# Kernel tuning notes

Hardware: AMD Instinct MI355X
Metric: run time of the kernel (lower is better)

Reference implementation:

```python
import jax, jax.numpy as jnp
import numpy as np

WH, WW = 7, 7
N = WH * WW
DIM = 384
HEADS = 12
NW = 64          # windows per image
B_ = 2048        # batch * NW


def _relative_position_index():
    ch, cw = np.meshgrid(np.arange(WH), np.arange(WW), indexing='ij')
    coords = np.stack([ch, cw]).reshape(2, -1)                      # [2, N]
    rel = coords[:, :, None] - coords[:, None, :]                   # [2, N, N]
    rel = rel.transpose(1, 2, 0)
    rel[:, :, 0] += WH - 1
    rel[:, :, 1] += WW - 1
    rel[:, :, 0] *= 2 * WW - 1
    return jnp.asarray(rel.sum(-1), dtype=jnp.int32)                # [N, N]


def setup_inputs() -> dict:
    key = jax.random.key(0)
    ks = jax.random.split(key, 7)
    return {
        'x': jax.random.normal(ks[0], (B_, N, DIM), dtype=jnp.float32),
        'qkv_w': jax.random.normal(ks[1], (3 * DIM, DIM), dtype=jnp.float32) * 0.02,
        'qkv_b': jax.random.normal(ks[2], (3 * DIM,), dtype=jnp.float32) * 0.02,
        'proj_w': jax.random.normal(ks[3], (DIM, DIM), dtype=jnp.float32) * 0.02,
        'proj_b': jax.random.normal(ks[4], (DIM,), dtype=jnp.float32) * 0.02,
        'bias_table': jax.random.normal(ks[5], ((2 * WH - 1) * (2 * WW - 1), HEADS), dtype=jnp.float32) * 0.02,
        'mask': jax.random.normal(ks[6], (NW, N, N), dtype=jnp.float32),
        'rel_idx': _relative_position_index(),
    }


def reference(x, qkv_w, qkv_b, proj_w, proj_b, bias_table, mask, rel_idx):
    B_, n, C = x.shape
    H = HEADS
    hd = C // H
    scale = hd ** (-0.5)

    qkv = x @ qkv_w.T + qkv_b                                        # [B_, N, 3C]
    qkv = qkv.reshape(B_, n, 3, H, hd).transpose(2, 0, 3, 1, 4)      # [3, B_, H, N, hd]
    q, k, v = qkv[0], qkv[1], qkv[2]

    attn = jnp.einsum('bhqd,bhkd->bhqk', q * scale, k)               # [B_, H, N, N]

    rpb = bias_table[rel_idx.reshape(-1)].reshape(n, n, H)           # gather [N, N, H]
    attn = attn + rpb.transpose(2, 0, 1)[None]                       # [B_, H, N, N]

    nW = mask.shape[0]
    attn = attn.reshape(B_ // nW, nW, H, n, n) + mask[None, :, None]
    attn = attn.reshape(B_, H, n, n)
    attn = jax.nn.softmax(attn, axis=-1)

    out = jnp.einsum('bhqk,bhkd->bhqd', attn, v)                     # [B_, H, N, hd]
    out = out.transpose(0, 2, 1, 3).reshape(B_, n, C)
    return out @ proj_w.T + proj_b
```

## Files before the change

kernel.cpp:

```cpp
#include <hip/hip_runtime.h>
#include <hip/hip_bf16.h>
#include <cstdint>
#include <cstddef>

#define NTOK 49
#define DIM 384
#define KDIM 384
#define HEADS 12
#define HD 32
#define BATCH 2048
#define MROWS (BATCH * NTOK)

typedef unsigned short u16;
typedef __bf16 bf16x8 __attribute__((ext_vector_type(8)));
typedef unsigned short u16x8 __attribute__((ext_vector_type(8)));
typedef float f32x4 __attribute__((ext_vector_type(4)));

__device__ __forceinline__ u16 f2b(float f) {
  union { float f; unsigned u; } v; v.f = f;
  unsigned r = v.u + 0x7fffu + ((v.u >> 16) & 1u);
  return (u16)(r >> 16);
}

__device__ __forceinline__ bf16x8 ld_bf8(const u16* p) {
  u16x8 u = *(const u16x8*)p;
  return __builtin_bit_cast(bf16x8, u);
}

__device__ __forceinline__ void gload_lds16(const void* g, void* l) {
  __builtin_amdgcn_global_load_lds(
      (const __attribute__((address_space(1))) unsigned*)g,
      (__attribute__((address_space(3))) unsigned*)l, 16, 0, 0);
}

__global__ __launch_bounds__(256) void k_prep(const float* __restrict__ x,
                                              u16* __restrict__ xb,
                                              const float* __restrict__ qkv_w,
                                              u16* __restrict__ wqkvb,
                                              const float* __restrict__ proj_w,
                                              u16* __restrict__ wprojb,
                                              const float* __restrict__ bias_table,
                                              const float* __restrict__ mask,
                                              const int* __restrict__ rel_idx,
                                              float* __restrict__ rpbm) {
  int blk = blockIdx.x;
  if (blk < 38208) {
    const float* in;
    u16* out;
    int i;
    if (blk < 37632) {
      in = x; out = xb; i = blk * 256 + threadIdx.x;
    } else if (blk < 38064) {
      in = qkv_w; out = wqkvb; i = (blk - 37632) * 256 + threadIdx.x;
    } else {
      in = proj_w; out = wprojb; i = (blk - 38064) * 256 + threadIdx.x;
    }
    float4 v = ((const float4*)in)[i];
    ushort4 o;
    o.x = f2b(v.x); o.y = f2b(v.y); o.z = f2b(v.z); o.w = f2b(v.w);
    ((ushort4*)out)[i] = o;
  } else {
    int idx = (blk - 38208) * 256 + threadIdx.x;
    int r  = idx & 3;
    int l  = (idx >> 2) & 63;
    int ni = (idx >> 8) & 3;
    int mi = (idx >> 10) & 3;
    int w  = (idx >> 12) & 63;
    int h  = idx >> 18;
    int kk = mi * 16 + (l >> 4) * 4 + r;
    int qq = ni * 16 + (l & 15);
    float v = -1e30f;
    if (kk < NTOK && qq < NTOK)
      v = bias_table[rel_idx[qq * NTOK + kk] * HEADS + h] +
          mask[(w * NTOK + qq) * NTOK + kk];
    rpbm[idx] = v;
  }
}

template <int OUT_BF16, int NCOLS, int NTN, int GD8>
__global__ __launch_bounds__(512, 4) void k_gemm256(const u16* __restrict__ A,
                                                    const u16* __restrict__ B,
                                                    const float* __restrict__ bias,
                                                    void* __restrict__ Cv) {
  __shared__ u16 sh[36864];
  int bid = blockIdx.x;
  int tile = (bid & 7) * GD8 + (bid >> 3);
  int mt = tile / NTN, nt = tile - mt * NTN;
  long m0 = (long)mt * 256;
  int n0 = nt * 128;
  int tid = threadIdx.x;
  int lane = tid & 63, wid = tid >> 6;
  int wr = (wid >> 1) * 64, wc = (wid & 1) * 64;
  int c = lane & 15, g = lane >> 4;
  int gsw = (g ^ ((c >> 1) & 3)) * 8;

  int srow = wid * 16 + (lane >> 2);
  int scol = ((lane & 3) ^ ((lane >> 3) & 3)) * 8;
  const u16* gA = A + (m0 + srow) * (long)KDIM + scol;
  const u16* gB = B + (long)(n0 + srow) * KDIM + scol;
  int lrow = srow, lseg = (lane & 3) * 8;

  f32x4 acc[4][4] = {};
  bf16x8 af[4], bfr[4];

#define STAGE256(BUF, KT)                                                      \
  {                                                                            \
    u16* As_ = sh + (BUF) * 12288;                                             \
    u16* Bs_ = As_ + 8192;                                                     \
    gload_lds16(gA + (KT), &As_[lrow * 32 + lseg]);                            \
    gload_lds16(gA + (KT) + 128L * KDIM, &As_[(lrow + 128) * 32 + lseg]);      \
    gload_lds16(gB + (KT), &Bs_[lrow * 32 + lseg]);                            \
  }

#define FRAGREAD(BUF)                                                          \
  {                                                                            \
    const u16* As = sh + (BUF) * 12288;                                        \
    const u16* Bs = As + 8192;                                                 \
    _Pragma("unroll") for (int i = 0; i < 4; ++i) {                            \
      af[i]  = ld_bf8(&As[(wr + i * 16 + c) * 32 + gsw]);                      \
      bfr[i] = ld_bf8(&Bs[(wc + i * 16 + c) * 32 + gsw]);                      \
    }                                                                          \
  }

#define MFMA_CL                                                                \
  __builtin_amdgcn_s_setprio(1);                                               \
  _Pragma("unroll") for (int mi = 0; mi < 4; ++mi)                             \
  _Pragma("unroll") for (int ni = 0; ni < 4; ++ni)                             \
      acc[mi][ni] = __builtin_amdgcn_mfma_f32_16x16x32_bf16(                   \
          af[mi], bfr[ni], acc[mi][ni], 0, 0, 0);                              \
  __builtin_amdgcn_s_setprio(0);

#define GITER(T, NV)                                                           \
  {                                                                            \
    MFMA_CL;                                                                   \
    asm volatile("s_waitcnt vmcnt(" #NV ")" ::: "memory");                     \
    __builtin_amdgcn_s_barrier();                                              \
    __builtin_amdgcn_sched_barrier(0);                                         \
    if ((T) + 3 < 12) STAGE256((T) % 3, ((T) + 3) * 32);                       \
    FRAGREAD(((T) + 1) % 3);                                                   \
  }

  STAGE256(0, 0);
  STAGE256(1, 32);
  STAGE256(2, 64);
  asm volatile("s_waitcnt vmcnt(6)" ::: "memory");
  __builtin_amdgcn_s_barrier();
  __builtin_amdgcn_sched_barrier(0);
  FRAGREAD(0);

  GITER(0, 3)  GITER(1, 3)  GITER(2, 3)  GITER(3, 3)
  GITER(4, 3)  GITER(5, 3)  GITER(6, 3)  GITER(7, 3)
  GITER(8, 3)  GITER(9, 3)  GITER(10, 0)
  { MFMA_CL; }
  __builtin_amdgcn_s_barrier();
#undef GITER
#undef MFMA_CL
#undef FRAGREAD
#undef STAGE256

  if (OUT_BF16) {
    u16* C = (u16*)Cv;
#pragma unroll
    for (int mi = 0; mi < 4; ++mi)
#pragma unroll
      for (int ni = 0; ni < 4; ++ni) {
        int col = wc + ni * 16 + c;
        float bv = bias[n0 + col];
#pragma unroll
        for (int r = 0; r < 4; ++r) {
          int row = wr + mi * 16 + g * 4 + r;
          sh[row * 128 + col] = f2b(acc[mi][ni][r] + bv);
        }
      }
    __syncthreads();
#pragma unroll
    for (int rep = 0; rep < 8; ++rep) {
      int idx = rep * 4096 + tid * 8;
      int row = idx >> 7, col = idx & 127;
      *(u16x8*)(C + (m0 + row) * NCOLS + n0 + col) = *(const u16x8*)&sh[idx];
    }
  } else {
    float* C = (float*)Cv;
    float* shf = (float*)sh;
#pragma unroll
    for (int chunk = 0; chunk < 2; ++chunk) {
      __syncthreads();
      if ((wid >> 2) == chunk) {
#pragma unroll
        for (int mi = 0; mi < 4; ++mi)
#pragma unroll
          for (int ni = 0; ni < 4; ++ni) {
            int col = wc + ni * 16 + c;
            float bv = bias[n0 + col];
#pragma unroll
            for (int r = 0; r < 4; ++r) {
              int lr = ((wid >> 1) & 1) * 64 + mi * 16 + g * 4 + r;
              shf[lr * 128 + col] = acc[mi][ni][r] + bv;
            }
          }
      }
      __syncthreads();
#pragma unroll
      for (int rep = 0; rep < 8; ++rep) {
        int idx = rep * 2048 + tid * 4;
        int row = idx >> 7, col = idx & 127;
        *(float4*)(C + (m0 + chunk * 128 + row) * NCOLS + n0 + col) =
            *(const float4*)&shf[idx];
      }
    }
  }
}

__global__ __launch_bounds__(256) void k_attn(const u16* __restrict__ qkv,
                                              const float* __restrict__ rpbmT,
                                              u16* __restrict__ attnout) {
  __shared__ u16 P_lds[4][64 * 64];
  __shared__ u16 vT_lds[4][32 * 64];
  int lane = threadIdx.x & 63, wid = threadIdx.x >> 6;
  int blk = blockIdx.x;
  int w = blk / 96;
  int rr = blk - w * 96;
  int j = rr / 3;
  int hb = rr - j * 3;
  int b = j * 64 + w;
  int h = hb * 4 + wid;
  const u16* base = qkv + (size_t)b * (NTOK * 1152);
  int c = lane & 15, g = lane >> 4;

  u16* vt = vT_lds[wid];
  {
    const u16* vbase = base + 2 * DIM + h * HD;
#pragma unroll
    for (int t = 0; t < 4; ++t) {
      int idx = t * 64 + lane;
      int jj = idx >> 2, d0 = (idx & 3) * 8;
      int jr = jj < NTOK ? jj : NTOK - 1;
      u16x8 vv = *(const u16x8*)(vbase + (size_t)jr * 1152 + d0);
#pragma unroll
      for (int dd = 0; dd < 8; ++dd) {
        int d = d0 + dd;
        int byte = (d * 128 + jj * 2) ^ ((d & 7) << 4);
        *(u16*)((char*)vt + byte) = (u16)vv[dd];
      }
    }
  }

  bf16x8 kf[4], qf[4];
#pragma unroll
  for (int mi = 0; mi < 4; ++mi) {
    int row = mi * 16 + c; if (row > NTOK - 1) row = NTOK - 1;
    kf[mi] = ld_bf8(base + (size_t)row * 1152 + DIM + h * HD + g * 8);
  }
#pragma unroll
  for (int nj = 0; nj < 4; ++nj) {
    int row = nj * 16 + c; if (row > NTOK - 1) row = NTOK - 1;
    qf[nj] = ld_bf8(base + (size_t)row * 1152 + h * HD + g * 8);
  }

  f32x4 s[4][4];
  f32x4 zf = {0.f, 0.f, 0.f, 0.f};
#pragma unroll
  for (int mi = 0; mi < 4; ++mi)
#pragma unroll
    for (int nj = 0; nj < 4; ++nj)
      s[mi][nj] = __builtin_amdgcn_mfma_f32_16x16x32_bf16(kf[mi], qf[nj], zf,
                                                          0, 0, 0);

  const float scale = 0.17677669529663687f;
  const f32x4* rp = (const f32x4*)(rpbmT + ((size_t)(h * 64 + w)) * 4096);
#pragma unroll
  for (int mi = 0; mi < 4; ++mi)
#pragma unroll
    for (int nj = 0; nj < 4; ++nj) {
      f32x4 rv = rp[(mi * 4 + nj) * 64 + lane];
#pragma unroll
      for (int r = 0; r < 4; ++r)
        s[mi][nj][r] = s[mi][nj][r] * scale + rv[r];
    }

  float inv[4];
#pragma unroll
  for (int nj = 0; nj < 4; ++nj) {
    float mx = s[0][nj][0];
#pragma unroll
    for (int mi = 0; mi < 4; ++mi)
#pragma unroll
      for (int r = 0; r < 4; ++r)
        mx = fmaxf(mx, s[mi][nj][r]);
    mx = fmaxf(mx, __shfl_xor(mx, 16));
    mx = fmaxf(mx, __shfl_xor(mx, 32));
    float sum = 0.f;
#pragma unroll
    for (int mi = 0; mi < 4; ++mi)
#pragma unroll
      for (int r = 0; r < 4; ++r) {
        float p = __expf(s[mi][nj][r] - mx);
        s[mi][nj][r] = p;
        sum += p;
      }
    sum += __shfl_xor(sum, 16);
    sum += __shfl_xor(sum, 32);
    inv[nj] = __builtin_amdgcn_rcpf(sum);
  }

  u16* pl = P_lds[wid];
#pragma unroll
  for (int mi = 0; mi < 4; ++mi)
#pragma unroll
    for (int nj = 0; nj < 4; ++nj) {
      unsigned w0, w1;
      asm("v_cvt_pk_bf16_f32 %0, %1, %2"
          : "=v"(w0) : "v"(s[mi][nj][0]), "v"(s[mi][nj][1]));
      asm("v_cvt_pk_bf16_f32 %0, %1, %2"
          : "=v"(w1) : "v"(s[mi][nj][2]), "v"(s[mi][nj][3]));
      int q = nj * 16 + c;
      int byte = (q * 128 + (mi * 16 + g * 4) * 2) ^ ((c & 7) << 4);
      uint2 val; val.x = w0; val.y = w1;
      *(uint2*)((char*)pl + byte) = val;
    }
  asm volatile("s_waitcnt lgkmcnt(0)" ::: "memory");
  __builtin_amdgcn_sched_barrier(0);

  f32x4 o[2][4] = {};
#pragma unroll
  for (int ks = 0; ks < 2; ++ks) {
    bf16x8 vb[2];
#pragma unroll
    for (int mi2 = 0; mi2 < 2; ++mi2) {
      int d = mi2 * 16 + c;
      int byte = (d * 128 + ks * 64 + g * 16) ^ ((d & 7) << 4);
      vb[mi2] = __builtin_bit_cast(bf16x8, *(const u16x8*)((const char*)vt + byte));
    }
#pragma unroll
    for (int nj = 0; nj < 4; ++nj) {
      int q = nj * 16 + c;
      int byte = (q * 128 + (ks * 32 + g * 8) * 2) ^ ((c & 7) << 4);
      bf16x8 pb = __builtin_bit_cast(bf16x8, *(const u16x8*)((const char*)pl + byte));
#pragma unroll
      for (int mi2 = 0; mi2 < 2; ++mi2)
        o[mi2][nj] = __builtin_amdgcn_mfma_f32_16x16x32_bf16(vb[mi2], pb,
                                                             o[mi2][nj], 0, 0, 0);
    }
  }

  u16* obase = attnout + (size_t)b * (NTOK * DIM) + h * HD;
#pragma unroll
  for (int mi2 = 0; mi2 < 2; ++mi2)
#pragma unroll
    for (int nj = 0; nj < 4; ++nj) {
      int q = nj * 16 + c;
      if (q < NTOK) {
#pragma unroll
        for (int r = 0; r < 4; ++r)
          obase[(size_t)q * DIM + mi2 * 16 + g * 4 + r] =
              f2b(o[mi2][nj][r] * inv[nj]);
      }
    }
}

extern "C" void kernel_launch(void* const* d_in, const int* in_sizes, int n_in,
                              void* d_out, int out_size, void* d_ws, size_t ws_size,
                              hipStream_t stream) {
  const float* x       = (const float*)d_in[0];
  const float* qkv_w   = (const float*)d_in[1];
  const float* qkv_b   = (const float*)d_in[2];
  const float* proj_w  = (const float*)d_in[3];
  const float* proj_b  = (const float*)d_in[4];
  const float* bias_tb = (const float*)d_in[5];
  const float* mask    = (const float*)d_in[6];
  const int*   rel_idx = (const int*)d_in[7];
  float* out = (float*)d_out;

  char* ws = (char*)d_ws;
  u16*   xb      = (u16*)(ws + 0);
  u16*   wqkvb   = (u16*)(ws + 77070336);
  u16*   wprojb  = (u16*)(ws + 77955072);
  float* rpbm    = (float*)(ws + 78249984);
  u16*   qkv     = (u16*)(ws + 90832896);
  u16*   attnout = (u16*)(ws + 322043904);

  k_prep<<<50496, 256, 0, stream>>>(x, xb, qkv_w, wqkvb, proj_w, wprojb,
                                    bias_tb, mask, rel_idx, rpbm);

  k_gemm256<1, 1152, 9, 441><<<3528, 512, 0, stream>>>(xb, wqkvb, qkv_b,
                                                       (void*)qkv);

  k_attn<<<6144, 256, 0, stream>>>(qkv, rpbm, attnout);

  k_gemm256<0, 384, 3, 147><<<1176, 512, 0, stream>>>(attnout, wprojb, proj_b,
                                                      (void*)out);

  (void)in_sizes; (void)n_in; (void)out_size; (void)ws_size;
}
```

Before: 341.7 us.

## Restructure GEMM main loop into 64-wide K tiles with quarter-phased double buffering

Replaces the 3-stage 32-wide K pipeline in the shared GEMM kernel with a 2-buffer, 64-wide K pipeline. Each K step is split into four quadrant phases of MFMA work, and the next tile's global-to-LDS loads are interleaved between phases with extra barriers. The LDS footprint grows and launch bounds drop to 2 blocks per CU, trading occupancy and added barriers for fewer loop iterations and finer overlap of loads with compute. The XOR swizzle is updated to match the 64-element row.

```diff
diff --git a/kernel.cpp b/kernel.cpp
--- a/kernel.cpp
+++ b/kernel.cpp
@@ -78,11 +78,11 @@
 }
 
 template <int OUT_BF16, int NCOLS, int NTN, int GD8>
-__global__ __launch_bounds__(512, 4) void k_gemm256(const u16* __restrict__ A,
-                                                    const u16* __restrict__ B,
-                                                    const float* __restrict__ bias,
-                                                    void* __restrict__ Cv) {
-  __shared__ u16 sh[36864];
+__global__ __launch_bounds__(512, 2) void k_gemm8p(const u16* __restrict__ A,
+                                                   const u16* __restrict__ B,
+                                                   const float* __restrict__ bias,
+                                                   void* __restrict__ Cv) {
+  __shared__ u16 sh[49152];
   int bid = blockIdx.x;
   int tile = (bid & 7) * GD8 + (bid >> 3);
   int mt = tile / NTN, nt = tile - mt * NTN;
@@ -92,71 +92,89 @@
   int lane = tid & 63, wid = tid >> 6;
   int wr = (wid >> 1) * 64, wc = (wid & 1) * 64;
   int c = lane & 15, g = lane >> 4;
-  int gsw = (g ^ ((c >> 1) & 3)) * 8;
-
-  int srow = wid * 16 + (lane >> 2);
-  int scol = ((lane & 3) ^ ((lane >> 3) & 3)) * 8;
-  const u16* gA = A + (m0 + srow) * (long)KDIM + scol;
-  const u16* gB = B + (long)(n0 + srow) * KDIM + scol;
-  int lrow = srow, lseg = (lane & 3) * 8;
+  int r8 = lane >> 3;
+  int sg = ((lane & 7) ^ r8) * 8;
+  const u16* gAb = A + (m0 + r8) * (long)KDIM + sg;
+  const u16* gBb = B + (long)(n0 + r8) * KDIM + sg;
+  int a_l0 = wid * 32;
+  int b_l0 = wid * 16;
 
   f32x4 acc[4][4] = {};
-  bf16x8 af[4], bfr[4];
-
-#define STAGE256(BUF, KT)                                                      \
+
+#define STA(BUF, KT, Q)                                                        \
+  gload_lds16(gAb + (long)(a_l0 + (Q) * 8) * KDIM + (KT),                      \
+              &sh[(BUF) * 24576 + (a_l0 + (Q) * 8) * 64] + lane * 8);
+#define STB(BUF, KT, Q)                                                        \
+  gload_lds16(gBb + (long)(b_l0 + (Q) * 8) * KDIM + (KT),                      \
+              &sh[(BUF) * 24576 + 16384 + (b_l0 + (Q) * 8) * 64] + lane * 8);
+
+#define READQ(BUF, MI0, NI0)                                                   \
+  const u16* As = sh + (BUF) * 24576;                                          \
+  const u16* Bs = As + 16384;                                                  \
+  bf16x8 aq[2][2], bq[2][2];                                                   \
+  _Pragma("unroll") for (int i = 0; i < 2; ++i) {                              \
+    int R = wr + ((MI0) + i) * 16 + c;                                         \
+    int S = wc + ((NI0) + i) * 16 + c;                                         \
+    _Pragma("unroll") for (int kk = 0; kk < 2; ++kk) {                         \
+      aq[i][kk] = ld_bf8(&As[R * 64 + (((kk * 4 + g) ^ (R & 7)) * 8)]);        \
+      bq[i][kk] = ld_bf8(&Bs[S * 64 + (((kk * 4 + g) ^ (S & 7)) * 8)]);        \
+    }                                                                          \
+  }
+
+#define MFMAQ(MI0, NI0)                                                        \
+  __builtin_amdgcn_s_setprio(1);                                               \
+  _Pragma("unroll") for (int kk = 0; kk < 2; ++kk)                             \
+  _Pragma("unroll") for (int i = 0; i < 2; ++i)                                \
+  _Pragma("unroll") for (int jj = 0; jj < 2; ++jj)                             \
+    acc[(MI0) + i][(NI0) + jj] = __builtin_amdgcn_mfma_f32_16x16x32_bf16(      \
+        aq[i][kk], bq[jj][kk], acc[(MI0) + i][(NI0) + jj], 0, 0, 0);           \
+  __builtin_amdgcn_s_setprio(0);
+
+#define GK(T, NV)                                                              \
   {                                                                            \
-    u16* As_ = sh + (BUF) * 12288;                                             \
-    u16* Bs_ = As_ + 8192;                                                     \
-    gload_lds16(gA + (KT), &As_[lrow * 32 + lseg]);                            \
-    gload_lds16(gA + (KT) + 128L * KDIM, &As_[(lrow + 128) * 32 + lseg]);      \
-    gload_lds16(gB + (KT), &Bs_[lrow * 32 + lseg]);                            \
-  }
-
-#define FRAGREAD(BUF)                                                          \
-  {                                                                            \
-    const u16* As = sh + (BUF) * 12288;                                        \
-    const u16* Bs = As + 8192;                                                 \
-    _Pragma("unroll") for (int i = 0; i < 4; ++i) {                            \
-      af[i]  = ld_bf8(&As[(wr + i * 16 + c) * 32 + gsw]);                      \
-      bfr[i] = ld_bf8(&Bs[(wc + i * 16 + c) * 32 + gsw]);                      \
-    }                                                                          \
-  }
-
-#define MFMA_CL                                                                \
-  __builtin_amdgcn_s_setprio(1);                                               \
-  _Pragma("unroll") for (int mi = 0; mi < 4; ++mi)                             \
-  _Pragma("unroll") for (int ni = 0; ni < 4; ++ni)                             \
-      acc[mi][ni] = __builtin_amdgcn_mfma_f32_16x16x32_bf16(                   \
-          af[mi], bfr[ni], acc[mi][ni], 0, 0, 0);                              \
-  __builtin_amdgcn_s_setprio(0);
-
-#define GITER(T, NV)                                                           \
-  {                                                                            \
-    MFMA_CL;                                                                   \
+    if ((T) + 1 < 6) { STA(((T) + 1) & 1, ((T) + 1) * 64, 0)                   \
+                       STA(((T) + 1) & 1, ((T) + 1) * 64, 1) }                 \
     asm volatile("s_waitcnt vmcnt(" #NV ")" ::: "memory");                     \
     __builtin_amdgcn_s_barrier();                                              \
     __builtin_amdgcn_sched_barrier(0);                                         \
-    if ((T) + 3 < 12) STAGE256((T) % 3, ((T) + 3) * 32);                       \
-    FRAGREAD(((T) + 1) % 3);                                                   \
-  }
-
-  STAGE256(0, 0);
-  STAGE256(1, 32);
-  STAGE256(2, 64);
-  asm volatile("s_waitcnt vmcnt(6)" ::: "memory");
-  __builtin_amdgcn_s_barrier();
-  __builtin_amdgcn_sched_barrier(0);
-  FRAGREAD(0);
-
-  GITER(0, 3)  GITER(1, 3)  GITER(2, 3)  GITER(3, 3)
-  GITER(4, 3)  GITER(5, 3)  GITER(6, 3)  GITER(7, 3)
-  GITER(8, 3)  GITER(9, 3)  GITER(10, 0)
-  { MFMA_CL; }
-  __builtin_amdgcn_s_barrier();
-#undef GITER
-#undef MFMA_CL
-#undef FRAGREAD
-#undef STAGE256
+    { READQ((T) & 1, 0, 0)                                                     \
+      asm volatile("s_waitcnt lgkmcnt(0)" ::: "memory");                       \
+      __builtin_amdgcn_sched_barrier(0);                                       \
+      MFMAQ(0, 0) }                                                            \
+    __builtin_amdgcn_s_barrier();                                              \
+    { READQ((T) & 1, 2, 0)                                                     \
+      if ((T) + 1 < 6) { STA(((T) + 1) & 1, ((T) + 1) * 64, 2)                 \
+                         STA(((T) + 1) & 1, ((T) + 1) * 64, 3) }               \
+      __builtin_amdgcn_s_barrier();                                            \
+      asm volatile("s_waitcnt lgkmcnt(0)" ::: "memory");                       \
+      __builtin_amdgcn_sched_barrier(0);                                       \
+      MFMAQ(2, 0) }                                                            \
+    __builtin_amdgcn_s_barrier();                                              \
+    { READQ((T) & 1, 0, 2)                                                     \
+      if ((T) + 1 < 6) { STB(((T) + 1) & 1, ((T) + 1) * 64, 0)                 \
+                         STB(((T) + 1) & 1, ((T) + 1) * 64, 1) }               \
+      __builtin_amdgcn_s_barrier();                                            \
+      asm volatile("s_waitcnt lgkmcnt(0)" ::: "memory");                       \
+      __builtin_amdgcn_sched_barrier(0);                                       \
+      MFMAQ(0, 2) }                                                            \
+    __builtin_amdgcn_s_barrier();                                              \
+    { READQ((T) & 1, 2, 2)                                                     \
+      __builtin_amdgcn_s_barrier();                                            \
+      asm volatile("s_waitcnt lgkmcnt(0)" ::: "memory");                       \
+      __builtin_amdgcn_sched_barrier(0);                                       \
+      MFMAQ(2, 2) }                                                            \
+    __builtin_amdgcn_s_barrier();                                              \
+  }
+
+  STA(0, 0, 0) STA(0, 0, 1) STA(0, 0, 2) STA(0, 0, 3)
+  STB(0, 0, 0) STB(0, 0, 1)
+
+  GK(0, 2) GK(1, 2) GK(2, 2) GK(3, 2) GK(4, 2) GK(5, 0)
+#undef GK
+#undef MFMAQ
+#undef READQ
+#undef STB
+#undef STA
 
   if (OUT_BF16) {
     u16* C = (u16*)Cv;
@@ -382,13 +400,13 @@
   k_prep<<<50496, 256, 0, stream>>>(x, xb, qkv_w, wqkvb, proj_w, wprojb,
                                     bias_tb, mask, rel_idx, rpbm);
 
-  k_gemm256<1, 1152, 9, 441><<<3528, 512, 0, stream>>>(xb, wqkvb, qkv_b,
-                                                       (void*)qkv);
+  k_gemm8p<1, 1152, 9, 441><<<3528, 512, 0, stream>>>(xb, wqkvb, qkv_b,
+                                                      (void*)qkv);
 
   k_attn<<<6144, 256, 0, stream>>>(qkv, rpbm, attnout);
 
-  k_gemm256<0, 384, 3, 147><<<1176, 512, 0, stream>>>(attnout, wprojb, proj_b,
-                                                      (void*)out);
+  k_gemm8p<0, 384, 3, 147><<<1176, 512, 0, stream>>>(attnout, wprojb, proj_b,
+                                                     (void*)out);
 
   (void)in_sizes; (void)n_in; (void)out_size; (void)ws_size;
 }
```

Measured after the change: 379.0 us. 1.11x slower.
